# Kernel optimization log

Hardware: AMD Instinct MI355X
Metric: run time of the kernel (lower is better)

The kernel has to match this reference:

```python
import jax, jax.numpy as jnp
import numpy as np

N = 50000
E = 800000
IN_C = 128
HID = 64
HEADS = 4
NEG_SLOPE = 0.2
EPS = 1e-16


def setup_inputs() -> dict:
    key = jax.random.key(0)
    ks = jax.random.split(key, 12)
    x = jax.random.normal(ks[0], (N, IN_C), dtype=jnp.float32)
    edge_index = jax.random.randint(ks[1], (2, E), 0, N, dtype=jnp.int64)
    # layer 1: in -> (HEADS, HID), concat heads
    W1 = jax.random.normal(ks[2], (IN_C, HEADS * HID), dtype=jnp.float32) * (1.0 / np.sqrt(IN_C))
    a_src1 = jax.random.normal(ks[3], (HEADS, HID), dtype=jnp.float32) * 0.1
    a_dst1 = jax.random.normal(ks[4], (HEADS, HID), dtype=jnp.float32) * 0.1
    b1 = jnp.zeros((HEADS * HID,), dtype=jnp.float32)
    # layer 2: HEADS*HID -> (1, HID)
    W2 = jax.random.normal(ks[5], (HEADS * HID, HID), dtype=jnp.float32) * (1.0 / np.sqrt(HEADS * HID))
    a_src2 = jax.random.normal(ks[6], (1, HID), dtype=jnp.float32) * 0.1
    a_dst2 = jax.random.normal(ks[7], (1, HID), dtype=jnp.float32) * 0.1
    b2 = jnp.zeros((HID,), dtype=jnp.float32)
    return {"x": x, "edge_index": edge_index, "W1": W1, "a_src1": a_src1,
            "a_dst1": a_dst1, "b1": b1, "W2": W2, "a_src2": a_src2,
            "a_dst2": a_dst2, "b2": b2}


def _gat_conv(x, src, dst, W, a_src, a_dst, bias, heads, ch):
    n = x.shape[0]
    h = (x @ W).reshape(n, heads, ch)                       # [N,H,C]
    alpha_s = jnp.einsum('nhc,hc->nh', h, a_src)            # [N,H]
    alpha_d = jnp.einsum('nhc,hc->nh', h, a_dst)            # [N,H]
    e = jax.nn.leaky_relu(alpha_s[src] + alpha_d[dst], NEG_SLOPE)  # [E,H]
    # segment softmax over incoming edges of each dst node
    m = jax.ops.segment_max(e, dst, num_segments=n)         # [N,H]
    ex = jnp.exp(e - m[dst])
    denom = jax.ops.segment_sum(ex, dst, num_segments=n)    # [N,H]
    alpha = ex / (denom[dst] + EPS)                         # [E,H]
    msg = h[src] * alpha[:, :, None]                        # [E,H,C]
    out = jax.ops.segment_sum(msg, dst, num_segments=n)     # [N,H,C]
    return out.reshape(n, heads * ch) + bias


def reference(x, edge_index, W1, a_src1, a_dst1, b1, W2, a_src2, a_dst2, b2):
    src = edge_index[0]
    dst = edge_index[1]
    h = _gat_conv(x, src, dst, W1, a_src1, a_dst1, b1, HEADS, HID)
    h = jax.nn.elu(h)
    h = _gat_conv(h, src, dst, W2, a_src2, a_dst2, b2, 1, HID)
    h = jax.nn.elu(h)
    return h  # [N, HID] (output_dim == hidden_channels so no final linear)
```

## Files before the change

kernel.cpp:

```cpp
#include <hip/hip_runtime.h>
#include <math.h>

#define NN 50000
#define EE 800000
#define IN_C 128
#define HID 64
#define HEADS 4
#define SCAN_BLOCKS ((NN + 255) / 256)
#define EBLOCKS ((EE + 255) / 256)
#define GEMM1B ((NN + 31) / 32)

typedef __attribute__((ext_vector_type(8))) short bf16x8;
typedef __attribute__((ext_vector_type(4))) float f32x4;

#if defined(__has_builtin)
#if __has_builtin(__builtin_amdgcn_fdot2_f32_bf16)
#define HAVE_FDOT2_BF16 1
#endif
#endif


__device__ inline unsigned short f2bf(float f) {
    unsigned u = __float_as_uint(f);
    return (unsigned short)((u + 0x7fff + ((u >> 16) & 1)) >> 16);
}
__device__ inline float bf2f(unsigned short s) {
    return __uint_as_float(((unsigned)s) << 16);
}
__device__ inline unsigned prm(unsigned a, unsigned b, unsigned sel) {
    return __builtin_amdgcn_perm(a, b, sel);
}
#ifdef HAVE_FDOT2_BF16
typedef __attribute__((ext_vector_type(2))) __bf16 bf2v;
__device__ inline float fdot2bf(unsigned h, unsigned w, float acc) {
    return __builtin_amdgcn_fdot2_f32_bf16(__builtin_bit_cast(bf2v, h),
                                           __builtin_bit_cast(bf2v, w), acc, false);
}
#else
__device__ inline float fdot2bf(unsigned h, unsigned w, float acc) {
    return acc + bf2f((unsigned short)(h & 0xffff)) * bf2f((unsigned short)(w & 0xffff))
               + bf2f((unsigned short)(h >> 16)) * bf2f((unsigned short)(w >> 16));
}
#endif

__device__ inline int wave_incl_scan(int v, int lane) {
    #pragma unroll
    for (int off = 1; off < 64; off <<= 1) {
        int t = __shfl_up(v, off);
        if (lane >= off) v += t;
    }
    return v;
}

__device__ inline int block256_excl_scan(int v, int tid, int* ws4) {
    int lane = tid & 63, wv = tid >> 6;
    int incl = wave_incl_scan(v, lane);
    if (lane == 63) ws4[wv] = incl;
    __syncthreads();
    if (tid == 0) {
        int run = 0;
        #pragma unroll
        for (int i = 0; i < 4; i++) { int t = ws4[i]; ws4[i] = run; run += t; }
    }
    __syncthreads();
    return incl + ws4[wv] - v;
}


__global__ void front_kernel(const int* __restrict__ ei, int* __restrict__ deg,
                             const float* __restrict__ W1, unsigned short* __restrict__ W1Thi,
                             unsigned short* __restrict__ W1Tlo,
                             const float* __restrict__ W2, unsigned short* __restrict__ W2Thi,
                             unsigned short* __restrict__ W2Tlo) {
    int b = blockIdx.x;
    int tid = threadIdx.x;
    if (b < EBLOCKS) {
        int i = b * 256 + tid;
        if (i < EE) atomicAdd(&deg[ei[EE + i]], 1);
    } else if (b < EBLOCKS + 128) {
        int idx = (b - EBLOCKS) * 256 + tid;
        int r = idx >> 8, c = idx & 255;
        float v = W1[idx];
        unsigned short h = f2bf(v);
        W1Thi[c * 128 + r] = h;
        W1Tlo[c * 128 + r] = f2bf(v - bf2f(h));
    } else {
        int idx = (b - EBLOCKS - 128) * 256 + tid;
        int r = idx >> 6, c = idx & 63;
        float v = W2[idx];
        unsigned short h = f2bf(v);
        W2Thi[c * 256 + r] = h;
        W2Tlo[c * 256 + r] = f2bf(v - bf2f(h));
    }
}


__global__ void deg_partial_kernel(const int* __restrict__ deg, int* __restrict__ bsum) {
    __shared__ int ws4[4];
    int tid = threadIdx.x;
    int idx = blockIdx.x * 256 + tid;
    int d = (idx < NN) ? deg[idx] : 0;
    int lane = tid & 63, wv = tid >> 6;
    int s = d;
    #pragma unroll
    for (int off = 32; off; off >>= 1) s += __shfl_down(s, off);
    if (lane == 0) ws4[wv] = s;
    __syncthreads();
    if (tid == 0) bsum[blockIdx.x] = ws4[0] + ws4[1] + ws4[2] + ws4[3];
}

__global__ void scanb_kernel(const int* __restrict__ bsum, int* __restrict__ boff,
                             int* __restrict__ row_ptr) {
    __shared__ int ws4[4];
    int tid = threadIdx.x;
    int v = (tid < SCAN_BLOCKS) ? bsum[tid] : 0;
    int excl = block256_excl_scan(v, tid, ws4);
    if (tid < SCAN_BLOCKS) boff[tid] = excl;
    if (tid == 255) row_ptr[NN] = excl + v;
}

__global__ void fill_kernel(const int* __restrict__ deg, const int* __restrict__ boff,
                            int* __restrict__ row_ptr, int* __restrict__ cursor) {
    __shared__ int ws4[4];
    int tid = threadIdx.x;
    int idx = blockIdx.x * 256 + tid;
    int d = (idx < NN) ? deg[idx] : 0;
    int excl = block256_excl_scan(d, tid, ws4) + boff[blockIdx.x];
    if (idx < NN) { row_ptr[idx] = excl; cursor[idx] = excl; }
}

__global__ __launch_bounds__(256) void scatter_gemm1_kernel(
        const int* __restrict__ ei, int* __restrict__ cursor, int* __restrict__ csr_src,
        const float* __restrict__ x,
        const unsigned short* __restrict__ Bhi, const unsigned short* __restrict__ Blo,
        const float* __restrict__ a_src, const float* __restrict__ a_dst,
        unsigned short* __restrict__ h1b, float* __restrict__ as1, float* __restrict__ ad1) {
    __shared__ unsigned short Ahi[32][136];
    __shared__ unsigned short Alo[32][136];
    int tid = threadIdx.x;
    if (blockIdx.x < EBLOCKS) {
        int i = blockIdx.x * 256 + tid;
        if (i < EE) {
            int d = ei[EE + i];
            int pos = atomicAdd(&cursor[d], 1);
            csr_src[pos] = ei[i];
        }
        return;
    }
    int w = tid >> 6, lane = tid & 63;
    int lq = lane >> 4, lr = lane & 15;
    int brow = (blockIdx.x - EBLOCKS) * 32;
    {
        int row = tid >> 3;
        int col0 = (tid & 7) * 16;
        int gr = min(brow + row, NN - 1);
        #pragma unroll
        for (int i = 0; i < 16; i += 4) {
            float4 v = *(const float4*)(x + (size_t)gr * 128 + col0 + i);
            unsigned short h0 = f2bf(v.x), h1 = f2bf(v.y), h2 = f2bf(v.z), h3 = f2bf(v.w);
            Ahi[row][col0 + i + 0] = h0; Alo[row][col0 + i + 0] = f2bf(v.x - bf2f(h0));
            Ahi[row][col0 + i + 1] = h1; Alo[row][col0 + i + 1] = f2bf(v.y - bf2f(h1));
            Ahi[row][col0 + i + 2] = h2; Alo[row][col0 + i + 2] = f2bf(v.z - bf2f(h2));
            Ahi[row][col0 + i + 3] = h3; Alo[row][col0 + i + 3] = f2bf(v.w - bf2f(h3));
        }
    }
    __syncthreads();
    f32x4 acc[2][4];
    f32x4 zf = {0.f, 0.f, 0.f, 0.f};
    #pragma unroll
    for (int mi = 0; mi < 2; mi++)
        #pragma unroll
        for (int ni = 0; ni < 4; ni++) acc[mi][ni] = zf;
    #pragma unroll
    for (int q = 0; q < 4; q++) {
        int ko = q * 32 + lq * 8;
        bf16x8 ah0 = *(const bf16x8*)(const void*)&Ahi[lr][ko];
        bf16x8 al0 = *(const bf16x8*)(const void*)&Alo[lr][ko];
        bf16x8 ah1 = *(const bf16x8*)(const void*)&Ahi[16 + lr][ko];
        bf16x8 al1 = *(const bf16x8*)(const void*)&Alo[16 + lr][ko];
        #pragma unroll
        for (int ni = 0; ni < 4; ni++) {
            size_t bo = (size_t)(w * 64 + ni * 16 + lr) * 128 + ko;
            bf16x8 bh = *(const bf16x8*)(const void*)(Bhi + bo);
            bf16x8 bl = *(const bf16x8*)(const void*)(Blo + bo);
            acc[0][ni] = __builtin_amdgcn_mfma_f32_16x16x32_bf16(al0, bh, acc[0][ni], 0, 0, 0);
            acc[0][ni] = __builtin_amdgcn_mfma_f32_16x16x32_bf16(ah0, bl, acc[0][ni], 0, 0, 0);
            acc[0][ni] = __builtin_amdgcn_mfma_f32_16x16x32_bf16(ah0, bh, acc[0][ni], 0, 0, 0);
            acc[1][ni] = __builtin_amdgcn_mfma_f32_16x16x32_bf16(al1, bh, acc[1][ni], 0, 0, 0);
            acc[1][ni] = __builtin_amdgcn_mfma_f32_16x16x32_bf16(ah1, bl, acc[1][ni], 0, 0, 0);
            acc[1][ni] = __builtin_amdgcn_mfma_f32_16x16x32_bf16(ah1, bh, acc[1][ni], 0, 0, 0);
        }
    }
    float asv[4], adv[4];
    #pragma unroll
    for (int ni = 0; ni < 4; ni++) {
        asv[ni] = a_src[w * 64 + ni * 16 + lr];
        adv[ni] = a_dst[w * 64 + ni * 16 + lr];
    }
    #pragma unroll
    for (int mi = 0; mi < 2; mi++) {
        f32x4 ps = zf, pd = zf;
        #pragma unroll
        for (int ni = 0; ni < 4; ni++)
            #pragma unroll
            for (int r = 0; r < 4; r++) {
                ps[r] += acc[mi][ni][r] * asv[ni];
                pd[r] += acc[mi][ni][r] * adv[ni];
            }
        #pragma unroll
        for (int m = 1; m < 16; m <<= 1)
            #pragma unroll
            for (int r = 0; r < 4; r++) {
                ps[r] += __shfl_xor(ps[r], m);
                pd[r] += __shfl_xor(pd[r], m);
            }
        #pragma unroll
        for (int r = 0; r < 4; r++) {
            int n = brow + mi * 16 + lq * 4 + r;
            if (lr == 0 && n < NN) { as1[n * 4 + w] = ps[r]; ad1[n * 4 + w] = pd[r]; }
        }
        #pragma unroll
        for (int ni = 0; ni < 4; ni++)
            #pragma unroll
            for (int r = 0; r < 4; r++) {
                int n = brow + mi * 16 + lq * 4 + r;
                if (n < NN)
                    h1b[(size_t)n * 256 + w * 64 + ni * 16 + lr] = f2bf(acc[mi][ni][r]);
            }
    }
}

__global__ __launch_bounds__(256) void gemm2_mfma(
        const unsigned short* __restrict__ Ahi, const unsigned short* __restrict__ Alo,
        const unsigned short* __restrict__ Bhi, const unsigned short* __restrict__ Blo,
        const float* __restrict__ a_src, const float* __restrict__ a_dst,
        unsigned short* __restrict__ g2b, float* __restrict__ as2, float* __restrict__ ad2) {
    int tid = threadIdx.x;
    int w = tid >> 6, lane = tid & 63;
    int lq = lane >> 4, lr = lane & 15;
    int wrow = blockIdx.x * 128 + w * 32;
    f32x4 acc[2][4];
    f32x4 zf = {0.f, 0.f, 0.f, 0.f};
    #pragma unroll
    for (int mi = 0; mi < 2; mi++)
        #pragma unroll
        for (int ni = 0; ni < 4; ni++) acc[mi][ni] = zf;
    int ra = min(wrow + lr, NN - 1);
    int rb = min(wrow + 16 + lr, NN - 1);
    #pragma unroll
    for (int q = 0; q < 8; q++) {
        int ko = q * 32 + lq * 8;
        bf16x8 ah0 = *(const bf16x8*)(const void*)(Ahi + (size_t)ra * 256 + ko);
        bf16x8 al0 = *(const bf16x8*)(const void*)(Alo + (size_t)ra * 256 + ko);
        bf16x8 ah1 = *(const bf16x8*)(const void*)(Ahi + (size_t)rb * 256 + ko);
        bf16x8 al1 = *(const bf16x8*)(const void*)(Alo + (size_t)rb * 256 + ko);
        #pragma unroll
        for (int ni = 0; ni < 4; ni++) {
            size_t bo = (size_t)(ni * 16 + lr) * 256 + ko;
            bf16x8 bh = *(const bf16x8*)(const void*)(Bhi + bo);
            bf16x8 bl = *(const bf16x8*)(const void*)(Blo + bo);
            acc[0][ni] = __builtin_amdgcn_mfma_f32_16x16x32_bf16(al0, bh, acc[0][ni], 0, 0, 0);
            acc[0][ni] = __builtin_amdgcn_mfma_f32_16x16x32_bf16(ah0, bl, acc[0][ni], 0, 0, 0);
            acc[0][ni] = __builtin_amdgcn_mfma_f32_16x16x32_bf16(ah0, bh, acc[0][ni], 0, 0, 0);
            acc[1][ni] = __builtin_amdgcn_mfma_f32_16x16x32_bf16(al1, bh, acc[1][ni], 0, 0, 0);
            acc[1][ni] = __builtin_amdgcn_mfma_f32_16x16x32_bf16(ah1, bl, acc[1][ni], 0, 0, 0);
            acc[1][ni] = __builtin_amdgcn_mfma_f32_16x16x32_bf16(ah1, bh, acc[1][ni], 0, 0, 0);
        }
    }
    float asv[4], adv[4];
    #pragma unroll
    for (int ni = 0; ni < 4; ni++) {
        asv[ni] = a_src[ni * 16 + lr];
        adv[ni] = a_dst[ni * 16 + lr];
    }
    #pragma unroll
    for (int mi = 0; mi < 2; mi++) {
        f32x4 ps = zf, pd = zf;
        #pragma unroll
        for (int ni = 0; ni < 4; ni++)
            #pragma unroll
            for (int r = 0; r < 4; r++) {
                ps[r] += acc[mi][ni][r] * asv[ni];
                pd[r] += acc[mi][ni][r] * adv[ni];
            }
        #pragma unroll
        for (int m = 1; m < 16; m <<= 1)
            #pragma unroll
            for (int r = 0; r < 4; r++) {
                ps[r] += __shfl_xor(ps[r], m);
                pd[r] += __shfl_xor(pd[r], m);
            }
        #pragma unroll
        for (int r = 0; r < 4; r++) {
            int n = wrow + mi * 16 + lq * 4 + r;
            if (lr == 0 && n < NN) { as2[n] = ps[r]; ad2[n] = pd[r]; }
        }
        #pragma unroll
        for (int ni = 0; ni < 4; ni++)
            #pragma unroll
            for (int r = 0; r < 4; r++) {
                int n = wrow + mi * 16 + lq * 4 + r;
                if (n < NN)
                    g2b[(size_t)n * 64 + ni * 16 + lr] = f2bf(acc[mi][ni][r]);
            }
    }
}

__global__ __launch_bounds__(256) void agg1_kernel(
        const unsigned short* __restrict__ h1b, const int* __restrict__ row_ptr,
        const int* __restrict__ csr_src, const float* __restrict__ as,
        const float* __restrict__ ad, const float* __restrict__ b1,
        unsigned short* __restrict__ h2hi, unsigned short* __restrict__ h2lo) {
    __shared__ int            ssrc[4][64];
    __shared__ unsigned short wbf[4][4][64];
    int tid = threadIdx.x;
    int wv = tid >> 6, lane = tid & 63;
    int n = blockIdx.x * 4 + wv;
    if (n >= NN) return;
    int start = row_ptr[n], end = row_ptr[n + 1];
    float4 adv = ((const float4*)ad)[n];
    int whead = lane >> 4;
    float4 acc = make_float4(0.f, 0.f, 0.f, 0.f);
    float d0 = 0.f, d1 = 0.f, d2 = 0.f, d3 = 0.f;
    for (int c0 = start; c0 < end; c0 += 64) {
        int m = min(64, end - c0);
        if (lane < m) {
            int s = csr_src[c0 + lane];
            ssrc[wv][lane] = s;
            float4 asv = ((const float4*)as)[s];
            float e0 = asv.x + adv.x; e0 = e0 > 0.f ? e0 : 0.2f * e0; float x0 = __expf(e0);
            float e1 = asv.y + adv.y; e1 = e1 > 0.f ? e1 : 0.2f * e1; float x1 = __expf(e1);
            float e2 = asv.z + adv.z; e2 = e2 > 0.f ? e2 : 0.2f * e2; float x2 = __expf(e2);
            float e3 = asv.w + adv.w; e3 = e3 > 0.f ? e3 : 0.2f * e3; float x3 = __expf(e3);
            wbf[wv][0][lane] = f2bf(x0);
            wbf[wv][1][lane] = f2bf(x1);
            wbf[wv][2][lane] = f2bf(x2);
            wbf[wv][3][lane] = f2bf(x3);
            d0 += x0; d1 += x1; d2 += x2; d3 += x3;
        }
        int j = 0;
        for (; j + 4 <= m; j += 4) {
            int s0 = ssrc[wv][j], s1 = ssrc[wv][j + 1];
            int s2 = ssrc[wv][j + 2], s3 = ssrc[wv][j + 3];
            uint2 ha = ((const uint2*)h1b)[(size_t)s0 * 64 + lane];
            uint2 hb = ((const uint2*)h1b)[(size_t)s1 * 64 + lane];
            uint2 hc = ((const uint2*)h1b)[(size_t)s2 * 64 + lane];
            uint2 hd = ((const uint2*)h1b)[(size_t)s3 * 64 + lane];
            unsigned wp01 = *(const unsigned*)&wbf[wv][whead][j];
            unsigned wp23 = *(const unsigned*)&wbf[wv][whead][j + 2];
            acc.x = fdot2bf(prm(hb.x, ha.x, 0x05040100), wp01, acc.x);
            acc.y = fdot2bf(prm(hb.x, ha.x, 0x07060302), wp01, acc.y);
            acc.z = fdot2bf(prm(hb.y, ha.y, 0x05040100), wp01, acc.z);
            acc.w = fdot2bf(prm(hb.y, ha.y, 0x07060302), wp01, acc.w);
            acc.x = fdot2bf(prm(hd.x, hc.x, 0x05040100), wp23, acc.x);
            acc.y = fdot2bf(prm(hd.x, hc.x, 0x07060302), wp23, acc.y);
            acc.z = fdot2bf(prm(hd.y, hc.y, 0x05040100), wp23, acc.z);
            acc.w = fdot2bf(prm(hd.y, hc.y, 0x07060302), wp23, acc.w);
        }
        for (; j + 2 <= m; j += 2) {
            int s0 = ssrc[wv][j], s1 = ssrc[wv][j + 1];
            uint2 ha = ((const uint2*)h1b)[(size_t)s0 * 64 + lane];
            uint2 hb = ((const uint2*)h1b)[(size_t)s1 * 64 + lane];
            unsigned wp = *(const unsigned*)&wbf[wv][whead][j];
            acc.x = fdot2bf(prm(hb.x, ha.x, 0x05040100), wp, acc.x);
            acc.y = fdot2bf(prm(hb.x, ha.x, 0x07060302), wp, acc.y);
            acc.z = fdot2bf(prm(hb.y, ha.y, 0x05040100), wp, acc.z);
            acc.w = fdot2bf(prm(hb.y, ha.y, 0x07060302), wp, acc.w);
        }
        if (j < m) {
            int s = ssrc[wv][j];
            float w = bf2f(wbf[wv][whead][j]);
            ushort4 hv = ((const ushort4*)h1b)[(size_t)s * 64 + lane];
            acc.x += bf2f(hv.x) * w; acc.y += bf2f(hv.y) * w;
            acc.z += bf2f(hv.z) * w; acc.w += bf2f(hv.w) * w;
        }
    }
    #pragma unroll
    for (int off = 32; off; off >>= 1) {
        d0 += __shfl_down(d0, off); d1 += __shfl_down(d1, off);
        d2 += __shfl_down(d2, off); d3 += __shfl_down(d3, off);
    }
    d0 = __shfl(d0, 0); d1 = __shfl(d1, 0);
    d2 = __shfl(d2, 0); d3 = __shfl(d3, 0);
    float den = whead == 0 ? d0 : whead == 1 ? d1 : whead == 2 ? d2 : d3;
    float inv = 1.f / (den + 1e-16f);
    float4 bv = ((const float4*)b1)[lane];
    float4 r;
    r.x = acc.x * inv + bv.x; r.y = acc.y * inv + bv.y;
    r.z = acc.z * inv + bv.z; r.w = acc.w * inv + bv.w;
    r.x = r.x > 0.f ? r.x : expm1f(r.x);
    r.y = r.y > 0.f ? r.y : expm1f(r.y);
    r.z = r.z > 0.f ? r.z : expm1f(r.z);
    r.w = r.w > 0.f ? r.w : expm1f(r.w);
    ushort4 hi4, lo4;
    hi4.x = f2bf(r.x); lo4.x = f2bf(r.x - bf2f(hi4.x));
    hi4.y = f2bf(r.y); lo4.y = f2bf(r.y - bf2f(hi4.y));
    hi4.z = f2bf(r.z); lo4.z = f2bf(r.z - bf2f(hi4.z));
    hi4.w = f2bf(r.w); lo4.w = f2bf(r.w - bf2f(hi4.w));
    ((ushort4*)h2hi)[(size_t)n * 64 + lane] = hi4;
    ((ushort4*)h2lo)[(size_t)n * 64 + lane] = lo4;
}

__global__ __launch_bounds__(256) void agg2_kernel(
        const unsigned short* __restrict__ g2b, const int* __restrict__ row_ptr,
        const int* __restrict__ csr_src, const float* __restrict__ as,
        const float* __restrict__ ad, const float* __restrict__ b2,
        float* __restrict__ out) {
    __shared__ int            ssrc[4][64];
    __shared__ unsigned short wbf[4][64];
    int tid = threadIdx.x;
    int wv = tid >> 6, lane = tid & 63;
    int n = blockIdx.x * 4 + wv;
    if (n >= NN) return;
    int start = row_ptr[n], end = row_ptr[n + 1];
    float adv = ad[n];
    float acc = 0.f;
    float den = 0.f;
    for (int c0 = start; c0 < end; c0 += 64) {
        int m = min(64, end - c0);
        if (lane < m) {
            int s = csr_src[c0 + lane];
            ssrc[wv][lane] = s;
            float e = as[s] + adv;
            e = e > 0.f ? e : 0.2f * e;
            float x = __expf(e);
            wbf[wv][lane] = f2bf(x);
            den += x;
        }
        int j = 0;
        for (; j + 4 <= m; j += 4) {
            int s0 = ssrc[wv][j], s1 = ssrc[wv][j + 1];
            int s2 = ssrc[wv][j + 2], s3 = ssrc[wv][j + 3];
            unsigned g0 = g2b[(size_t)s0 * 64 + lane];
            unsigned g1 = g2b[(size_t)s1 * 64 + lane];
            unsigned g2 = g2b[(size_t)s2 * 64 + lane];
            unsigned g3 = g2b[(size_t)s3 * 64 + lane];
            unsigned wp01 = *(const unsigned*)&wbf[wv][j];
            unsigned wp23 = *(const unsigned*)&wbf[wv][j + 2];
            acc = fdot2bf(prm(g1, g0, 0x05040100), wp01, acc);
            acc = fdot2bf(prm(g3, g2, 0x05040100), wp23, acc);
        }
        for (; j + 2 <= m; j += 2) {
            int s0 = ssrc[wv][j], s1 = ssrc[wv][j + 1];
            unsigned g0 = g2b[(size_t)s0 * 64 + lane];
            unsigned g1 = g2b[(size_t)s1 * 64 + lane];
            unsigned wp = *(const unsigned*)&wbf[wv][j];
            acc = fdot2bf(prm(g1, g0, 0x05040100), wp, acc);
        }
        if (j < m) {
            int s = ssrc[wv][j];
            acc += bf2f(g2b[(size_t)s * 64 + lane]) * bf2f(wbf[wv][j]);
        }
    }
    #pragma unroll
    for (int off = 32; off; off >>= 1) den += __shfl_down(den, off);
    den = __shfl(den, 0);
    float inv = 1.f / (den + 1e-16f);
    float r = acc * inv + b2[lane];
    out[(size_t)n * 64 + lane] = r > 0.f ? r : expm1f(r);
}


extern "C" void kernel_launch(void* const* d_in, const int* in_sizes, int n_in,
                              void* d_out, int out_size, void* d_ws, size_t ws_size,
                              hipStream_t stream) {
    const float* x      = (const float*)d_in[0];
    const int*   ei     = (const int*)d_in[1];
    const float* W1     = (const float*)d_in[2];
    const float* a_src1 = (const float*)d_in[3];
    const float* a_dst1 = (const float*)d_in[4];
    const float* b1     = (const float*)d_in[5];
    const float* W2     = (const float*)d_in[6];
    const float* a_src2 = (const float*)d_in[7];
    const float* a_dst2 = (const float*)d_in[8];
    const float* b2     = (const float*)d_in[9];
    float* out = (float*)d_out;

    char* base = (char*)d_ws;
    size_t off = 0;
    auto alloc = [&](size_t bytes) -> void* {
        void* p = base + off;
        off = (off + bytes + 255) & ~(size_t)255;
        return p;
    };
    int*   deg     = (int*)alloc(NN * sizeof(int));
    int*   bsum    = (int*)alloc(SCAN_BLOCKS * sizeof(int));
    int*   boff    = (int*)alloc(SCAN_BLOCKS * sizeof(int));
    int*   row_ptr = (int*)alloc((NN + 1) * sizeof(int));
    int*   cursor  = (int*)alloc(NN * sizeof(int));
    int*   csr_src = (int*)alloc(EE * sizeof(int));
    unsigned short* W1Thi = (unsigned short*)alloc(256 * 128 * 2);
    unsigned short* W1Tlo = (unsigned short*)alloc(256 * 128 * 2);
    unsigned short* W2Thi = (unsigned short*)alloc(64 * 256 * 2);
    unsigned short* W2Tlo = (unsigned short*)alloc(64 * 256 * 2);
    unsigned short* h1b   = (unsigned short*)alloc((size_t)NN * 256 * 2);
    float* as1     = (float*)alloc((size_t)NN * 4 * sizeof(float));
    float* ad1     = (float*)alloc((size_t)NN * 4 * sizeof(float));
    unsigned short* h2hi  = (unsigned short*)alloc((size_t)NN * 256 * 2);
    unsigned short* h2lo  = (unsigned short*)alloc((size_t)NN * 256 * 2);
    unsigned short* g2b   = (unsigned short*)alloc((size_t)NN * 64 * 2);
    float* as2     = (float*)alloc((size_t)NN * sizeof(float));
    float* ad2     = (float*)alloc((size_t)NN * sizeof(float));

    hipMemsetAsync(deg, 0, NN * sizeof(int), stream);

    front_kernel<<<EBLOCKS + 128 + 64, 256, 0, stream>>>(ei, deg, W1, W1Thi, W1Tlo,
                                                         W2, W2Thi, W2Tlo);
    deg_partial_kernel<<<SCAN_BLOCKS, 256, 0, stream>>>(deg, bsum);
    scanb_kernel<<<1, 256, 0, stream>>>(bsum, boff, row_ptr);
    fill_kernel<<<SCAN_BLOCKS, 256, 0, stream>>>(deg, boff, row_ptr, cursor);

    scatter_gemm1_kernel<<<EBLOCKS + GEMM1B, 256, 0, stream>>>(
        ei, cursor, csr_src, x, W1Thi, W1Tlo, a_src1, a_dst1, h1b, as1, ad1);

    agg1_kernel<<<(NN + 3) / 4, 256, 0, stream>>>(h1b, row_ptr, csr_src, as1, ad1, b1,
                                                  h2hi, h2lo);
    gemm2_mfma<<<(NN + 127) / 128, 256, 0, stream>>>(h2hi, h2lo, W2Thi, W2Tlo,
                                                     a_src2, a_dst2, g2b, as2, ad2);
    agg2_kernel<<<(NN + 3) / 4, 256, 0, stream>>>(g2b, row_ptr, csr_src, as2, ad2, b2, out);
}
```

Measured before the change: 342.5 us.

## Build CSR via atomic rank capture instead of second atomic cursor pass

The degree-counting atomic now records each edge's rank within its destination, so the later scatter writes csr_src[row_ptr[d]+rank[i]] with no second round of atomics on a cursor array. The scatter is split out of the fused scatter+GEMM1 kernel into its own launch, and GEMM1 becomes a standalone kernel. This removes the contended atomics in the scatter, at the cost of an extra E-sized rank buffer, more memory traffic, one extra kernel launch and the loss of overlap between the scatter and the GEMM.

```diff
diff --git a/kernel.cpp b/kernel.cpp
--- a/kernel.cpp
+++ b/kernel.cpp
@@ -8,7 +8,6 @@
 #define HEADS 4
 #define SCAN_BLOCKS ((NN + 255) / 256)
 #define EBLOCKS ((EE + 255) / 256)
-#define GEMM1B ((NN + 31) / 32)
 
 typedef __attribute__((ext_vector_type(8))) short bf16x8;
 typedef __attribute__((ext_vector_type(4))) float f32x4;
@@ -68,6 +67,7 @@
 
 
 __global__ void front_kernel(const int* __restrict__ ei, int* __restrict__ deg,
+                             int* __restrict__ rank,
                              const float* __restrict__ W1, unsigned short* __restrict__ W1Thi,
                              unsigned short* __restrict__ W1Tlo,
                              const float* __restrict__ W2, unsigned short* __restrict__ W2Thi,
@@ -76,7 +76,7 @@
     int tid = threadIdx.x;
     if (b < EBLOCKS) {
         int i = b * 256 + tid;
-        if (i < EE) atomicAdd(&deg[ei[EE + i]], 1);
+        if (i < EE) rank[i] = atomicAdd(&deg[ei[EE + i]], 1);
     } else if (b < EBLOCKS + 128) {
         int idx = (b - EBLOCKS) * 256 + tid;
         int r = idx >> 8, c = idx & 255;
@@ -120,17 +120,25 @@
 }
 
 __global__ void fill_kernel(const int* __restrict__ deg, const int* __restrict__ boff,
-                            int* __restrict__ row_ptr, int* __restrict__ cursor) {
+                            int* __restrict__ row_ptr) {
     __shared__ int ws4[4];
     int tid = threadIdx.x;
     int idx = blockIdx.x * 256 + tid;
     int d = (idx < NN) ? deg[idx] : 0;
     int excl = block256_excl_scan(d, tid, ws4) + boff[blockIdx.x];
-    if (idx < NN) { row_ptr[idx] = excl; cursor[idx] = excl; }
-}
-
-__global__ __launch_bounds__(256) void scatter_gemm1_kernel(
-        const int* __restrict__ ei, int* __restrict__ cursor, int* __restrict__ csr_src,
+    if (idx < NN) row_ptr[idx] = excl;
+}
+
+__global__ void scatter_kernel(const int* __restrict__ ei, const int* __restrict__ rank,
+                               const int* __restrict__ row_ptr, int* __restrict__ csr_src) {
+    int i = blockIdx.x * blockDim.x + threadIdx.x;
+    if (i < EE) {
+        int d = ei[EE + i];
+        csr_src[row_ptr[d] + rank[i]] = ei[i];
+    }
+}
+
+__global__ __launch_bounds__(256) void gemm1_mfma(
         const float* __restrict__ x,
         const unsigned short* __restrict__ Bhi, const unsigned short* __restrict__ Blo,
         const float* __restrict__ a_src, const float* __restrict__ a_dst,
@@ -138,18 +146,9 @@
     __shared__ unsigned short Ahi[32][136];
     __shared__ unsigned short Alo[32][136];
     int tid = threadIdx.x;
-    if (blockIdx.x < EBLOCKS) {
-        int i = blockIdx.x * 256 + tid;
-        if (i < EE) {
-            int d = ei[EE + i];
-            int pos = atomicAdd(&cursor[d], 1);
-            csr_src[pos] = ei[i];
-        }
-        return;
-    }
     int w = tid >> 6, lane = tid & 63;
     int lq = lane >> 4, lr = lane & 15;
-    int brow = (blockIdx.x - EBLOCKS) * 32;
+    int brow = blockIdx.x * 32;
     {
         int row = tid >> 3;
         int col0 = (tid & 7) * 16;
@@ -484,10 +483,10 @@
         return p;
     };
     int*   deg     = (int*)alloc(NN * sizeof(int));
+    int*   rank    = (int*)alloc(EE * sizeof(int));
     int*   bsum    = (int*)alloc(SCAN_BLOCKS * sizeof(int));
     int*   boff    = (int*)alloc(SCAN_BLOCKS * sizeof(int));
     int*   row_ptr = (int*)alloc((NN + 1) * sizeof(int));
-    int*   cursor  = (int*)alloc(NN * sizeof(int));
     int*   csr_src = (int*)alloc(EE * sizeof(int));
     unsigned short* W1Thi = (unsigned short*)alloc(256 * 128 * 2);
     unsigned short* W1Tlo = (unsigned short*)alloc(256 * 128 * 2);
@@ -504,15 +503,15 @@
 
     hipMemsetAsync(deg, 0, NN * sizeof(int), stream);
 
-    front_kernel<<<EBLOCKS + 128 + 64, 256, 0, stream>>>(ei, deg, W1, W1Thi, W1Tlo,
+    front_kernel<<<EBLOCKS + 128 + 64, 256, 0, stream>>>(ei, deg, rank, W1, W1Thi, W1Tlo,
                                                          W2, W2Thi, W2Tlo);
     deg_partial_kernel<<<SCAN_BLOCKS, 256, 0, stream>>>(deg, bsum);
     scanb_kernel<<<1, 256, 0, stream>>>(bsum, boff, row_ptr);
-    fill_kernel<<<SCAN_BLOCKS, 256, 0, stream>>>(deg, boff, row_ptr, cursor);
-
-    scatter_gemm1_kernel<<<EBLOCKS + GEMM1B, 256, 0, stream>>>(
-        ei, cursor, csr_src, x, W1Thi, W1Tlo, a_src1, a_dst1, h1b, as1, ad1);
-
+    fill_kernel<<<SCAN_BLOCKS, 256, 0, stream>>>(deg, boff, row_ptr);
+    scatter_kernel<<<EBLOCKS, 256, 0, stream>>>(ei, rank, row_ptr, csr_src);
+
+    gemm1_mfma<<<(NN + 31) / 32, 256, 0, stream>>>(x, W1Thi, W1Tlo,
+                                                   a_src1, a_dst1, h1b, as1, ad1);
     agg1_kernel<<<(NN + 3) / 4, 256, 0, stream>>>(h1b, row_ptr, csr_src, as1, ad1, b1,
                                                   h2hi, h2lo);
     gemm2_mfma<<<(NN + 127) / 128, 256, 0, stream>>>(h2hi, h2lo, W2Thi, W2Tlo,
```

Result: faster. 291.9 us (-14.8%).
